# Optimization experiments

Measured on AMD Instinct MI355X. Metric: run time of the kernel, lower is better.

The kernel has to match this reference:

```python
import jax, jax.numpy as jnp
import numpy as np

PAD_IDX = 0
VOCAB = 60
HIDDEN = 128
BATCH = 1024
SEQ = 256


def setup_inputs() -> dict:
    key = jax.random.key(0)
    ks = jax.random.split(key, 6)
    x = jax.random.randint(ks[0], (BATCH, SEQ), 0, VOCAB, dtype=jnp.int64 if jax.config.jax_enable_x64 else jnp.int32)
    lengths = jax.random.randint(ks[1], (BATCH,), 1, SEQ + 1, dtype=x.dtype)
    emb = jax.random.normal(ks[2], (VOCAB, HIDDEN), dtype=jnp.float32) * 0.1
    emb = emb.at[PAD_IDX].set(0.0)  # nn.Embedding padding_idx row is zero
    W_ih = jax.random.normal(ks[3], (HIDDEN, HIDDEN), dtype=jnp.float32) * (1.0 / np.sqrt(HIDDEN))
    W_hh = jax.random.normal(ks[4], (HIDDEN, HIDDEN), dtype=jnp.float32) * (1.0 / np.sqrt(HIDDEN))
    W_fc = jax.random.normal(ks[5], (VOCAB, HIDDEN), dtype=jnp.float32) * (1.0 / np.sqrt(HIDDEN))
    b_fc = jnp.zeros((VOCAB,), dtype=jnp.float32)
    return {"x": x, "lengths": lengths, "emb": emb, "W_ih": W_ih,
            "W_hh": W_hh, "W_fc": W_fc, "b_fc": b_fc}


def reference(x, lengths, emb, W_ih, W_hh, W_fc, b_fc):
    embedded = emb[x]                      # [B, T, H]
    B = embedded.shape[0]
    h0 = jnp.zeros((B, HIDDEN), dtype=embedded.dtype)

    def step(h_prev, x_t):
        # z_t = x_t @ W_ih^T + h_prev @ W_hh^T ; h_t = tanh(z_t)
        h_t = jnp.tanh(x_t @ W_ih.T + h_prev @ W_hh.T)
        return h_t, h_t

    _, hs = jax.lax.scan(step, h0, jnp.swapaxes(embedded, 0, 1))  # hs: [T, B, H]
    outputs = jnp.swapaxes(hs, 0, 1)       # [B, T, H]
    last_out = jnp.take_along_axis(outputs, (lengths - 1)[:, None, None], axis=1)[:, 0, :]  # [B, H]
    return last_out @ W_fc.T + b_fc[None, :]
```

## Files before the change

### kernel.cpp

```cpp
#include <hip/hip_runtime.h>
#include <hip/hip_bf16.h>

#define BATCH 1024
#define SEQ 256
#define HIDDEN 128
#define VOCAB 60
#define MTILE 16
#define ASTRIDE 136
#define XSTRIDE (SEQ + 1)

typedef _Float16 f16x8 __attribute__((ext_vector_type(8)));
typedef _Float16 f16x4 __attribute__((ext_vector_type(4)));
typedef float f32x4 __attribute__((ext_vector_type(4)));

__device__ __forceinline__ float fast_tanh(float x) {
    float e = __builtin_amdgcn_exp2f(x * 2.8853900817779268f);
    return __builtin_fmaf(-2.0f, __builtin_amdgcn_rcpf(e + 1.0f), 1.0f);
}

__global__ void rnn_prep_embw(const float* __restrict__ emb,
                              const float* __restrict__ W_ih,
                              float* __restrict__ embW) {
    const int v = blockIdx.x;
    const int i = threadIdx.x;
    __shared__ __align__(16) float e[HIDDEN];
    e[i] = emb[v * HIDDEN + i];
    __syncthreads();
    const float4* wrow = (const float4*)(W_ih + i * HIDDEN);
    const float4* e4 = (const float4*)e;
    float a0 = 0.f, a1 = 0.f, a2 = 0.f, a3 = 0.f;
#pragma unroll
    for (int j = 0; j < HIDDEN / 4; ++j) {
        float4 w = wrow[j];
        float4 h = e4[j];
        a0 += w.x * h.x; a1 += w.y * h.y; a2 += w.z * h.z; a3 += w.w * h.w;
    }
    embW[v * HIDDEN + i] = (a0 + a1) + (a2 + a3);
}

__global__ void __launch_bounds__(512)
rnn_mfma(const int* __restrict__ x, const int* __restrict__ lengths,
         const float* __restrict__ embW, const float* __restrict__ W_hh,
         const float* __restrict__ W_fc, const float* __restrict__ b_fc,
         float* __restrict__ out) {
    const int tid = threadIdx.x;
    const int wave = tid >> 6;
    const int lane = tid & 63;
    const int q = lane >> 4;
    const int r16 = lane & 15;
    const int c0 = wave * 16;
    const int b0 = blockIdx.x * MTILE;

    __shared__ __align__(16) _Float16 Ah[2][MTILE][ASTRIDE];
    __shared__ __align__(16) _Float16 ew[VOCAB][ASTRIDE];
    __shared__ int xs[MTILE][XSTRIDE];
    __shared__ __align__(16) float hfin[MTILE][HIDDEN];
    __shared__ int lenbuf[MTILE];

    for (int idx = tid; idx < MTILE * SEQ; idx += 512) {
        int r = idx >> 8, t = idx & (SEQ - 1);
        xs[r][t] = x[(b0 + r) * SEQ + t];
    }
    if (tid < MTILE) lenbuf[tid] = lengths[b0 + tid];
    for (int idx = tid; idx < VOCAB * HIDDEN; idx += 512) {
        int v = idx >> 7, c = idx & 127;
        ew[v][c] = (_Float16)embW[idx];
    }
    for (int idx = tid; idx < (int)(sizeof(Ah) / 4); idx += 512)
        ((int*)Ah)[idx] = 0;

    f16x8 Wf[4];
    {
        const float* wrow = W_hh + (c0 + r16) * HIDDEN + q * 8;
#pragma unroll
        for (int kc = 0; kc < 4; ++kc) {
            const float* p = wrow + kc * 32;
#pragma unroll
            for (int j = 0; j < 8; ++j) Wf[kc][j] = (_Float16)p[j];
        }
    }

    __syncthreads();

    const int mylen = lenbuf[r16];
    int lenmax = 0;
#pragma unroll
    for (int r = 0; r < MTILE; ++r) lenmax = max(lenmax, lenbuf[r]);

    int tok = xs[r16][0];
    f16x4 sd = *(const f16x4*)&ew[tok][c0 + 4 * q];

    int cur = 0;
    uint2 cap = {0u, 0u};

    for (int t = 0; t < lenmax; ++t) {
        const _Float16* hb = &Ah[cur][r16][q * 8];
        f16x8 H0 = *(const f16x8*)(hb + 0);
        f16x8 H1 = *(const f16x8*)(hb + 32);
        f16x8 H2 = *(const f16x8*)(hb + 64);
        f16x8 H3 = *(const f16x8*)(hb + 96);

        const int tn = (t + 1 < SEQ) ? t + 1 : SEQ - 1;
        const int tok1 = xs[r16][tn];
        f16x4 sn = *(const f16x4*)&ew[tok1][c0 + 4 * q];

        f32x4 a = {(float)sd[0], (float)sd[1], (float)sd[2], (float)sd[3]};
        f32x4 d = {0.f, 0.f, 0.f, 0.f};
        a = __builtin_amdgcn_mfma_f32_16x16x32_f16(Wf[0], H0, a, 0, 0, 0);
        d = __builtin_amdgcn_mfma_f32_16x16x32_f16(Wf[2], H2, d, 0, 0, 0);
        a = __builtin_amdgcn_mfma_f32_16x16x32_f16(Wf[1], H1, a, 0, 0, 0);
        d = __builtin_amdgcn_mfma_f32_16x16x32_f16(Wf[3], H3, d, 0, 0, 0);
        f32x4 z = a + d;

        float t0 = fast_tanh(z[0]);
        float t1 = fast_tanh(z[1]);
        float t2 = fast_tanh(z[2]);
        float t3 = fast_tanh(z[3]);

        uint2 pk;
        pk.x = __builtin_bit_cast(unsigned int, __builtin_amdgcn_cvt_pkrtz(t0, t1));
        pk.y = __builtin_bit_cast(unsigned int, __builtin_amdgcn_cvt_pkrtz(t2, t3));
        if (t + 1 == mylen) cap = pk;

        const int nxt = cur ^ 1;
        *(uint2*)&Ah[nxt][r16][c0 + 4 * q] = pk;
        __syncthreads();
        cur = nxt;
        sd = sn;
    }

    {
        f16x4 hc = __builtin_bit_cast(f16x4, cap);
#pragma unroll
        for (int v = 0; v < 4; ++v)
            hfin[r16][c0 + 4 * q + v] = (float)hc[v];
    }
    __syncthreads();

    const int r = tid >> 5;
    const int vb = tid & 31;
    const float4* hv = (const float4*)hfin[r];
    for (int vo = vb; vo < VOCAB; vo += 32) {
        const float4* wf = (const float4*)(W_fc + vo * HIDDEN);
        float a0 = 0.f, a1 = 0.f, a2 = 0.f, a3 = 0.f;
#pragma unroll
        for (int j = 0; j < HIDDEN / 4; ++j) {
            float4 a = hv[j];
            float4 w = wf[j];
            a0 += a.x * w.x; a1 += a.y * w.y; a2 += a.z * w.z; a3 += a.w * w.w;
        }
        out[(b0 + r) * VOCAB + vo] = (a0 + a1) + (a2 + a3) + b_fc[vo];
    }
}

extern "C" void kernel_launch(void* const* d_in, const int* in_sizes, int n_in,
                              void* d_out, int out_size, void* d_ws, size_t ws_size,
                              hipStream_t stream) {
    const int* x = (const int*)d_in[0];
    const int* lengths = (const int*)d_in[1];
    const float* emb = (const float*)d_in[2];
    const float* W_ih = (const float*)d_in[3];
    const float* W_hh = (const float*)d_in[4];
    const float* W_fc = (const float*)d_in[5];
    const float* b_fc = (const float*)d_in[6];
    float* out = (float*)d_out;

    float* embW = (float*)d_ws;

    rnn_prep_embw<<<VOCAB, HIDDEN, 0, stream>>>(emb, W_ih, embW);
    rnn_mfma<<<BATCH / MTILE, 512, 0, stream>>>(x, lengths, embW, W_hh, W_fc, b_fc, out);
}
```

Baseline: 175.3 us.

## Shrink batch tile to 4 rows per block to spread work across more CUs

Each block now handles 4 batch rows instead of 16, so the grid grows from 64 to 256 blocks and the serial recurrence is spread over more compute units. The MFMA tile is still 16 wide, so lanes map rows modulo 4 and only the first 4 rows write the hidden state. This wastes most of the MFMA throughput per block in exchange for more parallelism across the device. The change also prefetches the token index two steps ahead, keeps the captured final state in fp32 instead of fp16, and gives one thread to each output logit in the final projection.

```diff
diff --git a/kernel.cpp b/kernel.cpp
--- a/kernel.cpp
+++ b/kernel.cpp
@@ -5,9 +5,9 @@
 #define SEQ 256
 #define HIDDEN 128
 #define VOCAB 60
-#define MTILE 16
+#define ROWS 4
 #define ASTRIDE 136
-#define XSTRIDE (SEQ + 1)
+#define EWSTRIDE 132
 
 typedef _Float16 f16x8 __attribute__((ext_vector_type(8)));
 typedef _Float16 f16x4 __attribute__((ext_vector_type(4)));
@@ -48,24 +48,25 @@
     const int lane = tid & 63;
     const int q = lane >> 4;
     const int r16 = lane & 15;
+    const int r4 = r16 & 3;
     const int c0 = wave * 16;
-    const int b0 = blockIdx.x * MTILE;
+    const int b0 = blockIdx.x * ROWS;
 
-    __shared__ __align__(16) _Float16 Ah[2][MTILE][ASTRIDE];
-    __shared__ __align__(16) _Float16 ew[VOCAB][ASTRIDE];
-    __shared__ int xs[MTILE][XSTRIDE];
-    __shared__ __align__(16) float hfin[MTILE][HIDDEN];
-    __shared__ int lenbuf[MTILE];
+    __shared__ __align__(16) _Float16 Ah[2][ROWS][ASTRIDE];
+    __shared__ __align__(16) _Float16 ew[VOCAB][EWSTRIDE];
+    __shared__ int xs[ROWS][SEQ + 1];
+    __shared__ __align__(16) float hfin[ROWS][HIDDEN];
+    __shared__ int lenbuf[ROWS];
 
-    for (int idx = tid; idx < MTILE * SEQ; idx += 512) {
-        int r = idx >> 8, t = idx & (SEQ - 1);
-        xs[r][t] = x[(b0 + r) * SEQ + t];
-    }
-    if (tid < MTILE) lenbuf[tid] = lengths[b0 + tid];
     for (int idx = tid; idx < VOCAB * HIDDEN; idx += 512) {
         int v = idx >> 7, c = idx & 127;
         ew[v][c] = (_Float16)embW[idx];
     }
+    for (int idx = tid; idx < ROWS * SEQ; idx += 512) {
+        int r = idx >> 8, t = idx & (SEQ - 1);
+        xs[r][t] = x[(b0 + r) * SEQ + t];
+    }
+    if (tid < ROWS) lenbuf[tid] = lengths[b0 + tid];
     for (int idx = tid; idx < (int)(sizeof(Ah) / 4); idx += 512)
         ((int*)Ah)[idx] = 0;
 
@@ -82,27 +83,28 @@
 
     __syncthreads();
 
-    const int mylen = lenbuf[r16];
+    const int mylen = lenbuf[r4];
     int lenmax = 0;
 #pragma unroll
-    for (int r = 0; r < MTILE; ++r) lenmax = max(lenmax, lenbuf[r]);
+    for (int r = 0; r < ROWS; ++r) lenmax = max(lenmax, lenbuf[r]);
 
-    int tok = xs[r16][0];
+    int tok = xs[r4][0];
     f16x4 sd = *(const f16x4*)&ew[tok][c0 + 4 * q];
+    int tok1 = xs[r4][1];
 
     int cur = 0;
-    uint2 cap = {0u, 0u};
+    f32x4 cap = {0.f, 0.f, 0.f, 0.f};
 
     for (int t = 0; t < lenmax; ++t) {
-        const _Float16* hb = &Ah[cur][r16][q * 8];
+        const _Float16* hb = &Ah[cur][r4][q * 8];
         f16x8 H0 = *(const f16x8*)(hb + 0);
         f16x8 H1 = *(const f16x8*)(hb + 32);
         f16x8 H2 = *(const f16x8*)(hb + 64);
         f16x8 H3 = *(const f16x8*)(hb + 96);
 
-        const int tn = (t + 1 < SEQ) ? t + 1 : SEQ - 1;
-        const int tok1 = xs[r16][tn];
         f16x4 sn = *(const f16x4*)&ew[tok1][c0 + 4 * q];
+        const int t2 = (t + 2 < SEQ) ? t + 2 : SEQ - 1;
+        const int tok2 = xs[r4][t2];
 
         f32x4 a = {(float)sd[0], (float)sd[1], (float)sd[2], (float)sd[3]};
         f32x4 d = {0.f, 0.f, 0.f, 0.f};
@@ -112,44 +114,43 @@
         d = __builtin_amdgcn_mfma_f32_16x16x32_f16(Wf[3], H3, d, 0, 0, 0);
         f32x4 z = a + d;
 
-        float t0 = fast_tanh(z[0]);
-        float t1 = fast_tanh(z[1]);
-        float t2 = fast_tanh(z[2]);
-        float t3 = fast_tanh(z[3]);
+        f32x4 th;
+        th[0] = fast_tanh(z[0]);
+        th[1] = fast_tanh(z[1]);
+        th[2] = fast_tanh(z[2]);
+        th[3] = fast_tanh(z[3]);
+        if (t + 1 == mylen) cap = th;
 
         uint2 pk;
-        pk.x = __builtin_bit_cast(unsigned int, __builtin_amdgcn_cvt_pkrtz(t0, t1));
-        pk.y = __builtin_bit_cast(unsigned int, __builtin_amdgcn_cvt_pkrtz(t2, t3));
-        if (t + 1 == mylen) cap = pk;
+        pk.x = __builtin_bit_cast(unsigned int, __builtin_amdgcn_cvt_pkrtz(th[0], th[1]));
+        pk.y = __builtin_bit_cast(unsigned int, __builtin_amdgcn_cvt_pkrtz(th[2], th[3]));
 
         const int nxt = cur ^ 1;
-        *(uint2*)&Ah[nxt][r16][c0 + 4 * q] = pk;
+        if (r16 < ROWS)
+            *(uint2*)&Ah[nxt][r16][c0 + 4 * q] = pk;
         __syncthreads();
         cur = nxt;
         sd = sn;
+        tok1 = tok2;
     }
 
-    {
-        f16x4 hc = __builtin_bit_cast(f16x4, cap);
-#pragma unroll
-        for (int v = 0; v < 4; ++v)
-            hfin[r16][c0 + 4 * q + v] = (float)hc[v];
-    }
+    if (r16 < ROWS)
+        *(f32x4*)&hfin[r16][c0 + 4 * q] = cap;
     __syncthreads();
 
-    const int r = tid >> 5;
-    const int vb = tid & 31;
-    const float4* hv = (const float4*)hfin[r];
-    for (int vo = vb; vo < VOCAB; vo += 32) {
-        const float4* wf = (const float4*)(W_fc + vo * HIDDEN);
+    const int r = tid >> 7;
+    const int c = tid & 127;
+    if (c < VOCAB) {
+        const float4* hv = (const float4*)hfin[r];
+        const float4* wf = (const float4*)(W_fc + c * HIDDEN);
         float a0 = 0.f, a1 = 0.f, a2 = 0.f, a3 = 0.f;
 #pragma unroll
         for (int j = 0; j < HIDDEN / 4; ++j) {
-            float4 a = hv[j];
+            float4 h = hv[j];
             float4 w = wf[j];
-            a0 += a.x * w.x; a1 += a.y * w.y; a2 += a.z * w.z; a3 += a.w * w.w;
+            a0 += h.x * w.x; a1 += h.y * w.y; a2 += h.z * w.z; a3 += h.w * w.w;
         }
-        out[(b0 + r) * VOCAB + vo] = (a0 + a1) + (a2 + a3) + b_fc[vo];
+        out[(b0 + r) * VOCAB + c] = (a0 + a1) + (a2 + a3) + b_fc[c];
     }
 }
 
@@ -168,5 +169,5 @@
     float* embW = (float*)d_ws;
 
     rnn_prep_embw<<<VOCAB, HIDDEN, 0, stream>>>(emb, W_ih, embW);
-    rnn_mfma<<<BATCH / MTILE, 512, 0, stream>>>(x, lengths, embW, W_hh, W_fc, b_fc, out);
+    rnn_mfma<<<BATCH / ROWS, 512, 0, stream>>>(x, lengths, embW, W_hh, W_fc, b_fc, out);
 }
```

New measurement: 173.7 us. About the same (-0.9%).
